# Optimization experiments

Measured on AMD Instinct MI355X. Metric: run time of the kernel, lower is better.

## Reference

```python
import jax, jax.numpy as jnp
import numpy as np

N = 50000      # nodes
E = 400000     # edges
F_NODE = 16    # node_features
F_EDGE = 8     # edge_features
H = 16         # hidden_dim
HID_MLP = 32   # edge-MLP hidden width (from MLP([edge_features, 32, ...]))
G = 64         # graphs in batch
T = 2          # num_targets
EPS = 1e-5


def setup_inputs() -> dict:
    key = jax.random.key(0)
    ks = jax.random.split(key, 16)
    def nrm(k, shape, s=0.05):
        return jax.random.normal(k, shape, jnp.float32) * s
    z = lambda *s: jnp.zeros(s, jnp.float32)
    o = lambda *s: jnp.ones(s, jnp.float32)
    inp = {}
    inp['x'] = jax.random.normal(ks[0], (N, F_NODE), jnp.float32)
    inp['edge_attr'] = jax.random.normal(ks[1], (E, F_EDGE), jnp.float32)
    # conv1 edge-MLP: Linear(F_EDGE,32) -> BN -> ReLU -> Linear(32, F_NODE*H)
    inp['e1_W1'] = nrm(ks[2], (F_EDGE, HID_MLP)); inp['e1_b1'] = z(HID_MLP)
    inp['e1_g'] = o(HID_MLP); inp['e1_be'] = z(HID_MLP)
    inp['e1_W2'] = nrm(ks[3], (HID_MLP, F_NODE * H)); inp['e1_b2'] = z(F_NODE * H)
    inp['c1_root'] = nrm(ks[4], (F_NODE, H)); inp['c1_bias'] = z(H)
    # conv2 edge-MLP: Linear(F_EDGE,32) -> BN -> ReLU -> Linear(32, H*H)
    inp['e2_W1'] = nrm(ks[5], (F_EDGE, HID_MLP)); inp['e2_b1'] = z(HID_MLP)
    inp['e2_g'] = o(HID_MLP); inp['e2_be'] = z(HID_MLP)
    inp['e2_W2'] = nrm(ks[6], (HID_MLP, H * H)); inp['e2_b2'] = z(H * H)
    inp['c2_root'] = nrm(ks[7], (H, H)); inp['c2_bias'] = z(H)
    # node batch norms
    inp['bn1_g'] = o(H); inp['bn1_b'] = z(H)
    inp['bn2_g'] = o(H); inp['bn2_b'] = z(H)
    # head MLP
    inp['fc1_W'] = nrm(ks[8], (H, H)); inp['fc1_b'] = z(H)
    inp['fc2_W'] = nrm(ks[9], (H, T)); inp['fc2_b'] = z(T)
    # int args
    inp['edge_index'] = jax.random.randint(ks[10], (2, E), 0, N, dtype=jnp.int32).astype(jnp.int64)
    inp['batch'] = jnp.sort(jax.random.randint(ks[11], (N,), 0, G, dtype=jnp.int32)).astype(jnp.int64)
    return inp


def _bn(h, g, b):
    # training-mode BatchNorm1d: batch stats, biased variance
    m = h.mean(0)
    v = jnp.mean((h - m) ** 2, axis=0)
    return g * (h - m) / jnp.sqrt(v + EPS) + b


def _edge_mlp(e, W1, b1, g, be, W2, b2):
    h = jax.nn.relu(_bn(e @ W1 + b1, g, be))
    return h @ W2 + b2


def _seg_mean(vals, idx, num):
    s = jax.ops.segment_sum(vals, idx, num_segments=num)
    c = jax.ops.segment_sum(jnp.ones((idx.shape[0],), vals.dtype), idx, num_segments=num)
    return s / jnp.maximum(c, 1.0)[:, None]


def _nnconv(x, src, dst, e, W1, b1, g, be, W2, b2, Wroot, bias, in_c, out_c):
    w = _edge_mlp(e, W1, b1, g, be, W2, b2).reshape(-1, in_c, out_c)  # [E, in, out]
    msg = jnp.einsum('ei,eio->eo', x[src], w)                        # gather + per-edge matmul
    agg = _seg_mean(msg, dst, x.shape[0])                            # scatter-mean into targets
    return agg + x @ Wroot + bias


def reference(x, edge_attr, e1_W1, e1_b1, e1_g, e1_be, e1_W2, e1_b2, c1_root, c1_bias,
              e2_W1, e2_b1, e2_g, e2_be, e2_W2, e2_b2, c2_root, c2_bias,
              bn1_g, bn1_b, bn2_g, bn2_b, fc1_W, fc1_b, fc2_W, fc2_b,
              edge_index, batch):
    src, dst = edge_index[0], edge_index[1]
    h = _nnconv(x, src, dst, edge_attr, e1_W1, e1_b1, e1_g, e1_be, e1_W2, e1_b2,
                c1_root, c1_bias, F_NODE, H)
    h = jax.nn.relu(_bn(h, bn1_g, bn1_b))
    h = _nnconv(h, src, dst, edge_attr, e2_W1, e2_b1, e2_g, e2_be, e2_W2, e2_b2,
                c2_root, c2_bias, H, H)
    h = jax.nn.relu(_bn(h, bn2_g, bn2_b))
    pooled = _seg_mean(h, batch, G)          # global_mean_pool -> [G, H]
    out = jax.nn.relu(pooled @ fc1_W + fc1_b) @ fc2_W + fc2_b
    return out
```

## Files before the change

### kernel.cpp

```cpp
#include <hip/hip_runtime.h>

#define N_NODES 50000
#define N_EDGES 400000
#define NG 64
#define NT 2
#define EPS 1e-5f
#define NB_N ((N_NODES + 255) / 256)
#define NB_E ((N_EDGES + 255) / 256)
#define NB_A ((N_NODES + 31) / 32)

constexpr int mom_i(int t) {
    int tt = t - 8; int i = 0;
    while (tt >= 8 - i) { tt -= 8 - i; ++i; }
    return i;
}
constexpr int mom_j(int t) {
    int tt = t - 8; int i = 0;
    while (tt >= 8 - i) { tt -= 8 - i; ++i; }
    return i + tt;
}

template<int IDX>
__device__ __forceinline__ float mom_term(const float* v) {
    if constexpr (IDX >= 44) return 0.f;
    else if constexpr (IDX < 8) return v[IDX];
    else return v[mom_i(IDX)] * v[mom_j(IDX)];
}

template<int BASE>
__device__ __forceinline__ void mom_add(const float* v, float* acc) {
    acc[0] += mom_term<BASE + 0>(v);
    acc[1] += mom_term<BASE + 1>(v);
    acc[2] += mom_term<BASE + 2>(v);
    acc[3] += mom_term<BASE + 3>(v);
    acc[4] += mom_term<BASE + 4>(v);
    acc[5] += mom_term<BASE + 5>(v);
    acc[6] += mom_term<BASE + 6>(v);
    acc[7] += mom_term<BASE + 7>(v);
}

template<int BASE>
__device__ __forceinline__ void mom_loop(
    const float* __restrict__ ea, const int* __restrict__ dst,
    int* __restrict__ deg, float* acc)
{
    const int stride = gridDim.x * 256;
    for (int e = blockIdx.x * 256 + threadIdx.x; e < N_EDGES; e += stride) {
        const float4 a4 = ((const float4*)ea)[e * 2];
        const float4 b4 = ((const float4*)ea)[e * 2 + 1];
        const float v[8] = {a4.x,a4.y,a4.z,a4.w, b4.x,b4.y,b4.z,b4.w};
        if constexpr (BASE == 0) atomicAdd(deg + dst[e], 1);
        mom_add<BASE>(v, acc);
    }
}

__global__ __launch_bounds__(256) void k_moments(
    const float* __restrict__ ea, const int* __restrict__ dst,
    float* __restrict__ mom, int* __restrict__ deg)
{
    const int c = blockIdx.y;
    float acc[8] = {0.f,0.f,0.f,0.f,0.f,0.f,0.f,0.f};
    switch (c) {
        case 0: mom_loop<0 >(ea, dst, deg, acc); break;
        case 1: mom_loop<8 >(ea, dst, deg, acc); break;
        case 2: mom_loop<16>(ea, dst, deg, acc); break;
        case 3: mom_loop<24>(ea, dst, deg, acc); break;
        case 4: mom_loop<32>(ea, dst, deg, acc); break;
        default: mom_loop<40>(ea, dst, deg, acc); break;
    }
    __shared__ float red[4][8];
    const int lane = threadIdx.x & 63, wv = threadIdx.x >> 6;
    #pragma unroll
    for (int u = 0; u < 8; ++u) {
        float s = acc[u];
        #pragma unroll
        for (int o = 32; o; o >>= 1) s += __shfl_down(s, o);
        if (lane == 0) red[wv][u] = s;
    }
    __syncthreads();
    if (threadIdx.x < 8) {
        const int idx = c * 8 + threadIdx.x;
        if (idx < 44) {
            const float s = red[0][threadIdx.x] + red[1][threadIdx.x]
                          + red[2][threadIdx.x] + red[3][threadIdx.x];
            atomicAdd(mom + idx, s);
        }
    }
}

__global__ __launch_bounds__(256) void k_scan1(
    const int* __restrict__ deg, int* __restrict__ loc, int* __restrict__ bsum,
    int* __restrict__ hist)
{
    __shared__ int s[256];
    __shared__ int shist[128];
    const int t = threadIdx.x;
    const int n = blockIdx.x * 256 + t;
    const int v = (n < N_NODES) ? deg[n] : 0;
    if (t < 128) shist[t] = 0;
    s[t] = v;
    __syncthreads();
    #pragma unroll
    for (int d = 1; d < 256; d <<= 1) {
        const int a = (t >= d) ? s[t - d] : 0;
        __syncthreads();
        s[t] += a;
        __syncthreads();
    }
    if (n < N_NODES) {
        loc[n] = s[t] - v;
        atomicAdd(&shist[min(v, 127)], 1);
    }
    if (t == 255) bsum[blockIdx.x] = s[t];
    __syncthreads();
    if (t < 128 && shist[t]) atomicAdd(hist + t, shist[t]);
}

__global__ __launch_bounds__(256) void k_singles(
    int* __restrict__ bsum, const float* __restrict__ mom,
    const float* __restrict__ W1a, const float* __restrict__ b1a,
    const float* __restrict__ ga,  const float* __restrict__ bea,
    const float* __restrict__ W1b, const float* __restrict__ b1b,
    const float* __restrict__ gb,  const float* __restrict__ beb,
    float* __restrict__ ss, const int* __restrict__ batch,
    int* __restrict__ start, const int* __restrict__ hist,
    int* __restrict__ cursor)
{
    __shared__ int s[256];
    const int t = threadIdx.x;
    const int v = (t < NB_N) ? bsum[t] : 0;
    s[t] = v;
    __syncthreads();
    #pragma unroll
    for (int d = 1; d < 256; d <<= 1) {
        const int a = (t >= d) ? s[t - d] : 0;
        __syncthreads();
        s[t] += a;
        __syncthreads();
    }
    if (t < NB_N) bsum[t] = s[t] - v;

    if (t < 64) {
        const int m = t >> 5, k = t & 31;
        const float* W1 = m ? W1b : W1a;
        const float b   = (m ? b1b : b1a)[k];
        const float g   = (m ? gb  : ga)[k];
        const float be  = (m ? beb : bea)[k];
        float w[8];
        #pragma unroll
        for (int j = 0; j < 8; ++j) w[j] = W1[j * 32 + k];
        float Sw = 0.f;
        #pragma unroll
        for (int j = 0; j < 8; ++j) Sw += mom[j] * w[j];
        float q = 0.f;
        int idx = 8;
        #pragma unroll
        for (int i = 0; i < 8; ++i)
            #pragma unroll
            for (int j = i; j < 8; ++j) {
                const float Mv = mom[idx++];
                q += Mv * w[i] * w[j] * (i == j ? 1.f : 2.f);
            }
        const float invE  = 1.0f / (float)N_EDGES;
        const float sump  = Sw + (float)N_EDGES * b;
        const float sumpp = q + 2.f * b * Sw + (float)N_EDGES * b * b;
        const float mean  = sump * invE;
        const float var   = fmaxf(sumpp * invE - mean * mean, 0.f);
        const float sc    = g * rsqrtf(var + EPS);
        ss[m * 64 + k]      = sc;
        ss[m * 64 + 32 + k] = be - mean * sc;
    }
    if (t <= NG) {
        int lo = 0, hi = N_NODES;
        while (lo < hi) {
            const int mid = (lo + hi) >> 1;
            if (batch[mid] < t) lo = mid + 1; else hi = mid;
        }
        start[t] = lo;
    }
    if (t == 0) {
        int acc = 0;
        for (int d = 127; d >= 0; --d) { cursor[d] = acc; acc += hist[d]; }
    }
}

__global__ __launch_bounds__(256) void k_scan3(
    const int* __restrict__ loc, const int* __restrict__ bsum,
    const int* __restrict__ deg, int* __restrict__ off, int* __restrict__ cur,
    int* __restrict__ cursor, int* __restrict__ perm)
{
    __shared__ int scnt[128];
    __shared__ int sbase[128];
    const int t = threadIdx.x;
    const int n = blockIdx.x * 256 + t;
    if (t < 128) scnt[t] = 0;
    __syncthreads();
    int b = 0, rk = 0;
    if (n < N_NODES) {
        const int o = loc[n] + bsum[n >> 8];
        off[n] = o; cur[n] = o;
        if (n == 0) off[N_NODES] = N_EDGES;
        b  = min(deg[n], 127);
        rk = atomicAdd(&scnt[b], 1);
    }
    __syncthreads();
    if (t < 128 && scnt[t]) sbase[t] = atomicAdd(cursor + t, scnt[t]);
    __syncthreads();
    if (n < N_NODES) perm[sbase[b] + rk] = n;
}

__global__ __launch_bounds__(256) void k_pos(
    const int* __restrict__ src, const int* __restrict__ dst,
    const float* __restrict__ ea, int* __restrict__ cur,
    int* __restrict__ src_s, float4* __restrict__ ea_s)
{
    const int e = blockIdx.x * 256 + threadIdx.x;
    if (e < N_EDGES) {
        const float4 a4 = ((const float4*)ea)[e * 2];
        const float4 b4 = ((const float4*)ea)[e * 2 + 1];
        const int p = atomicAdd(cur + dst[e], 1);
        src_s[p] = src[e];
        ea_s[p * 2]     = a4;
        ea_s[p * 2 + 1] = b4;
    }
}

__global__ __launch_bounds__(256) void k_agg(
    const float* __restrict__ x, const float4* __restrict__ ea_s,
    const int* __restrict__ src_s, const int* __restrict__ off,
    const int* __restrict__ perm,
    const float* __restrict__ W1, const float* __restrict__ W2,
    const float* __restrict__ ss,
    float* __restrict__ agg_out, float* __restrict__ xsum_out)
{
    __shared__ float4 sW2q[2048];
    const int tid = threadIdx.x;
    #pragma unroll
    for (int i = 0; i < 8; ++i) {
        const int f = tid + 256 * i;
        sW2q[f ^ ((f >> 8) & 7)] = ((const float4*)W2)[f];
    }
    __syncthreads();

    const int c  = tid & 7;
    const int g  = blockIdx.x * 32 + (tid >> 3);
    if (g >= N_NODES) return;
    const int n  = perm[g];

    float w1r[32];
    #pragma unroll
    for (int j = 0; j < 8; ++j)
        #pragma unroll
        for (int kk = 0; kk < 4; ++kk)
            w1r[j * 4 + kk] = W1[j * 32 + c * 4 + kk];
    float scr[4], shr[4];
    #pragma unroll
    for (int kk = 0; kk < 4; ++kk) {
        scr[kk] = ss[c * 4 + kk];
        shr[kk] = ss[32 + c * 4 + kk];
    }

    const int o0 = off[n], o1 = off[n + 1];
    float T[64];
    #pragma unroll
    for (int j = 0; j < 64; ++j) T[j] = 0.f;
    float xs0 = 0.f, xs1 = 0.f;

    float4 ca, cb, cx0, cx1, cx2, cx3;
    if (o0 < o1) {
        const int sn = src_s[o0];
        ca = ea_s[(size_t)o0 * 2];
        cb = ea_s[(size_t)o0 * 2 + 1];
        const float4* xp = (const float4*)(x + (size_t)sn * 16);
        cx0 = xp[0]; cx1 = xp[1]; cx2 = xp[2]; cx3 = xp[3];
    }
    for (int r = o0; r < o1; ++r) {
        float4 na = ca, nb = cb, nx0 = cx0, nx1 = cx1, nx2 = cx2, nx3 = cx3;
        if (r + 1 < o1) {
            const int sn = src_s[r + 1];
            na = ea_s[(size_t)(r + 1) * 2];
            nb = ea_s[(size_t)(r + 1) * 2 + 1];
            const float4* xp = (const float4*)(x + (size_t)sn * 16);
            nx0 = xp[0]; nx1 = xp[1]; nx2 = xp[2]; nx3 = xp[3];
        }
        const float ein[8] = {ca.x,ca.y,ca.z,ca.w, cb.x,cb.y,cb.z,cb.w};
        float h[4];
        #pragma unroll
        for (int kk = 0; kk < 4; ++kk) {
            float p = 0.f;
            #pragma unroll
            for (int j = 0; j < 8; ++j) p += ein[j] * w1r[j * 4 + kk];
            h[kk] = fmaxf(p * scr[kk] + shr[kk], 0.f);
        }
        const float xv[16] = {cx0.x,cx0.y,cx0.z,cx0.w, cx1.x,cx1.y,cx1.z,cx1.w,
                              cx2.x,cx2.y,cx2.z,cx2.w, cx3.x,cx3.y,cx3.z,cx3.w};
        #pragma unroll
        for (int kk = 0; kk < 4; ++kk) {
            const float hk = h[kk];
            #pragma unroll
            for (int i = 0; i < 16; ++i) T[kk * 16 + i] += hk * xv[i];
        }
        xs0 += xv[c * 2];
        xs1 += xv[c * 2 + 1];
        ca = na; cb = nb; cx0 = nx0; cx1 = nx1; cx2 = nx2; cx3 = nx3;
    }

    float agg[16];
    #pragma unroll
    for (int o = 0; o < 16; ++o) agg[o] = 0.f;
    #pragma unroll
    for (int kk = 0; kk < 4; ++kk) {
        const int fbase = (c * 4 + kk) * 64;
        #pragma unroll
        for (int i = 0; i < 16; ++i) {
            const float tv = T[kk * 16 + i];
            const int f0 = fbase + i * 4;
            const float4 w0 = sW2q[(f0 + 0) ^ c];
            const float4 w1 = sW2q[(f0 + 1) ^ c];
            const float4 w2 = sW2q[(f0 + 2) ^ c];
            const float4 w3 = sW2q[(f0 + 3) ^ c];
            agg[0]+=tv*w0.x; agg[1]+=tv*w0.y; agg[2]+=tv*w0.z; agg[3]+=tv*w0.w;
            agg[4]+=tv*w1.x; agg[5]+=tv*w1.y; agg[6]+=tv*w1.z; agg[7]+=tv*w1.w;
            agg[8]+=tv*w2.x; agg[9]+=tv*w2.y; agg[10]+=tv*w2.z; agg[11]+=tv*w2.w;
            agg[12]+=tv*w3.x; agg[13]+=tv*w3.y; agg[14]+=tv*w3.z; agg[15]+=tv*w3.w;
        }
    }
    #pragma unroll
    for (int m = 1; m < 8; m <<= 1) {
        #pragma unroll
        for (int o = 0; o < 16; ++o) agg[o] += __shfl_xor(agg[o], m);
    }
    ((float2*)(agg_out  + (size_t)n * 16))[c] = make_float2(agg[c * 2], agg[c * 2 + 1]);
    ((float2*)(xsum_out + (size_t)n * 16))[c] = make_float2(xs0, xs1);
}

__global__ __launch_bounds__(256) void k_node_pre(
    const float* __restrict__ agg, const float* __restrict__ xsum,
    const int* __restrict__ off, const float* __restrict__ xin,
    const float* __restrict__ root, const float* __restrict__ b2,
    const float* __restrict__ bias, float* __restrict__ bnstats,
    float* __restrict__ pre_out)
{
    __shared__ float sroot[256], sb2[256], sbias[16], lacc[32];
    const int tid = threadIdx.x;
    if (tid < 64) {
        ((float4*)sroot)[tid] = ((const float4*)root)[tid];
        ((float4*)sb2)[tid]   = ((const float4*)b2)[tid];
    }
    if (tid < 16) sbias[tid] = bias[tid];
    if (tid < 32) lacc[tid] = 0.f;
    __syncthreads();

    const int n = blockIdx.x * 256 + tid;
    const bool valid = (n < N_NODES);
    float pre[16];
    if (valid) {
        float acc[16];
        const float4* ap = (const float4*)(agg + (size_t)n * 16);
        const float4 a0 = ap[0], a1 = ap[1], a2 = ap[2], a3 = ap[3];
        acc[0]=a0.x; acc[1]=a0.y; acc[2]=a0.z; acc[3]=a0.w;
        acc[4]=a1.x; acc[5]=a1.y; acc[6]=a1.z; acc[7]=a1.w;
        acc[8]=a2.x; acc[9]=a2.y; acc[10]=a2.z; acc[11]=a2.w;
        acc[12]=a3.x; acc[13]=a3.y; acc[14]=a3.z; acc[15]=a3.w;
        const float4* sp = (const float4*)(xsum + (size_t)n * 16);
        const float4 s0 = sp[0], s1 = sp[1], s2 = sp[2], s3 = sp[3];
        const float sv[16] = {s0.x,s0.y,s0.z,s0.w, s1.x,s1.y,s1.z,s1.w,
                              s2.x,s2.y,s2.z,s2.w, s3.x,s3.y,s3.z,s3.w};
        #pragma unroll
        for (int i = 0; i < 16; ++i) {
            const float si = sv[i];
            #pragma unroll
            for (int o = 0; o < 16; ++o) acc[o] += si * sb2[i * 16 + o];
        }
        const float inv = 1.0f / (float)max(off[n + 1] - off[n], 1);
        const float4* xp = (const float4*)(xin + (size_t)n * 16);
        const float4 x0=xp[0],x1=xp[1],x2=xp[2],x3=xp[3];
        const float xn[16] = {x0.x,x0.y,x0.z,x0.w, x1.x,x1.y,x1.z,x1.w,
                              x2.x,x2.y,x2.z,x2.w, x3.x,x3.y,x3.z,x3.w};
        #pragma unroll
        for (int o = 0; o < 16; ++o) pre[o] = sbias[o] + acc[o] * inv;
        #pragma unroll
        for (int i = 0; i < 16; ++i) {
            const float xi = xn[i];
            #pragma unroll
            for (int o = 0; o < 16; ++o) pre[o] += xi * sroot[i * 16 + o];
        }
        float4* wp4 = (float4*)(pre_out + (size_t)n * 16);
        wp4[0] = make_float4(pre[0],pre[1],pre[2],pre[3]);
        wp4[1] = make_float4(pre[4],pre[5],pre[6],pre[7]);
        wp4[2] = make_float4(pre[8],pre[9],pre[10],pre[11]);
        wp4[3] = make_float4(pre[12],pre[13],pre[14],pre[15]);
    } else {
        #pragma unroll
        for (int o = 0; o < 16; ++o) pre[o] = 0.f;
    }
    const int lane = tid & 63;
    #pragma unroll
    for (int o = 0; o < 16; ++o) {
        float s = pre[o], q = s * s;
        #pragma unroll
        for (int w = 32; w; w >>= 1) {
            s += __shfl_down(s, w);
            q += __shfl_down(q, w);
        }
        if (lane == 0) { atomicAdd(&lacc[o], s); atomicAdd(&lacc[16 + o], q); }
    }
    __syncthreads();
    if (tid < 32) atomicAdd(bnstats + tid, lacc[tid]);
}

__global__ __launch_bounds__(256) void k_node_bn(
    const float* __restrict__ pre, const float* __restrict__ bnstats,
    const float* __restrict__ gam, const float* __restrict__ bet,
    float* __restrict__ hout)
{
    __shared__ float sscale[16], sshift[16];
    const int tid = threadIdx.x;
    if (tid < 16) {
        const float mean = bnstats[tid] * (1.0f / N_NODES);
        const float var  = fmaxf(bnstats[16 + tid] * (1.0f / N_NODES) - mean * mean, 0.f);
        const float rs   = rsqrtf(var + EPS);
        const float sc   = gam[tid] * rs;
        sscale[tid] = sc;
        sshift[tid] = bet[tid] - mean * sc;
    }
    __syncthreads();
    const int n = blockIdx.x * 256 + tid;
    if (n >= N_NODES) return;
    const float4* pp = (const float4*)(pre + (size_t)n * 16);
    const float4 p0=pp[0],p1=pp[1],p2=pp[2],p3=pp[3];
    const float pv[16] = {p0.x,p0.y,p0.z,p0.w, p1.x,p1.y,p1.z,p1.w,
                          p2.x,p2.y,p2.z,p2.w, p3.x,p3.y,p3.z,p3.w};
    float h[16];
    #pragma unroll
    for (int o = 0; o < 16; ++o) h[o] = fmaxf(pv[o] * sscale[o] + sshift[o], 0.f);
    float4* hp = (float4*)(hout + (size_t)n * 16);
    hp[0] = make_float4(h[0],h[1],h[2],h[3]);
    hp[1] = make_float4(h[4],h[5],h[6],h[7]);
    hp[2] = make_float4(h[8],h[9],h[10],h[11]);
    hp[3] = make_float4(h[12],h[13],h[14],h[15]);
}

__global__ __launch_bounds__(256) void k_pool_bn(
    const float* __restrict__ pre, const float* __restrict__ bnstats,
    const float* __restrict__ gam, const float* __restrict__ bet,
    const int* __restrict__ start, float* __restrict__ pool)
{
    __shared__ float lds[16][16];
    __shared__ float sscale[16], sshift[16];
    const int tid = threadIdx.x;
    if (tid < 16) {
        const float mean = bnstats[tid] * (1.0f / N_NODES);
        const float var  = fmaxf(bnstats[16 + tid] * (1.0f / N_NODES) - mean * mean, 0.f);
        const float rs   = rsqrtf(var + EPS);
        const float sc   = gam[tid] * rs;
        sscale[tid] = sc;
        sshift[tid] = bet[tid] - mean * sc;
    }
    __syncthreads();
    const int g = blockIdx.x;
    const int c = tid & 15, rg = tid >> 4;
    const int s = start[g], e = start[g + 1];
    const float sc = sscale[c], sh = sshift[c];
    float acc = 0.f;
    for (int r = s + rg; r < e; r += 16)
        acc += fmaxf(pre[(size_t)r * 16 + c] * sc + sh, 0.f);
    lds[rg][c] = acc;
    __syncthreads();
    if (tid < 16) {
        float sum = 0.f;
        #pragma unroll
        for (int i = 0; i < 16; ++i) sum += lds[i][tid];
        const float inv = 1.0f / (float)max(e - s, 1);
        pool[g * 16 + tid] = sum * inv;
    }
}

__global__ __launch_bounds__(64) void k_head(
    const float* __restrict__ pool,
    const float* __restrict__ fc1W, const float* __restrict__ fc1b,
    const float* __restrict__ fc2W, const float* __restrict__ fc2b,
    float* __restrict__ out)
{
    const int g = threadIdx.x;
    if (g >= NG) return;
    float p[16];
    #pragma unroll
    for (int o = 0; o < 16; ++o) p[o] = pool[g * 16 + o];
    float z[16];
    #pragma unroll
    for (int j = 0; j < 16; ++j) {
        float a = fc1b[j];
        #pragma unroll
        for (int o = 0; o < 16; ++o) a += p[o] * fc1W[o * 16 + j];
        z[j] = fmaxf(a, 0.f);
    }
    #pragma unroll
    for (int t = 0; t < NT; ++t) {
        float a = fc2b[t];
        #pragma unroll
        for (int j = 0; j < 16; ++j) a += z[j] * fc2W[j * 2 + t];
        out[g * 2 + t] = a;
    }
}

extern "C" void kernel_launch(void* const* d_in, const int* in_sizes, int n_in,
                              void* d_out, int out_size, void* d_ws, size_t ws_size,
                              hipStream_t stream)
{
    const float* x    = (const float*)d_in[0];
    const float* ea   = (const float*)d_in[1];
    const float* e1W1 = (const float*)d_in[2];  const float* e1b1 = (const float*)d_in[3];
    const float* e1g  = (const float*)d_in[4];  const float* e1be = (const float*)d_in[5];
    const float* e1W2 = (const float*)d_in[6];  const float* e1b2 = (const float*)d_in[7];
    const float* c1r  = (const float*)d_in[8];  const float* c1b  = (const float*)d_in[9];
    const float* e2W1 = (const float*)d_in[10]; const float* e2b1 = (const float*)d_in[11];
    const float* e2g  = (const float*)d_in[12]; const float* e2be = (const float*)d_in[13];
    const float* e2W2 = (const float*)d_in[14]; const float* e2b2 = (const float*)d_in[15];
    const float* c2r  = (const float*)d_in[16]; const float* c2b  = (const float*)d_in[17];
    const float* bn1g = (const float*)d_in[18]; const float* bn1b = (const float*)d_in[19];
    const float* bn2g = (const float*)d_in[20]; const float* bn2b = (const float*)d_in[21];
    const float* fc1W = (const float*)d_in[22]; const float* fc1b = (const float*)d_in[23];
    const float* fc2W = (const float*)d_in[24]; const float* fc2b = (const float*)d_in[25];
    const int* eidx   = (const int*)d_in[26];
    const int* batch  = (const int*)d_in[27];
    const int* src = eidx;
    const int* dst = eidx + N_EDGES;

    float* ws      = (float*)d_ws;
    float* mom     = ws;
    float* bnstats = ws + 64;
    float* ss      = ws + 128;
    int* hist_i    = (int*)(ws + 256);
    int* cursor_i  = (int*)(ws + 384);
    int* deg_i   = (int*)(ws + 512);
    int* loc_i   = deg_i + N_NODES;
    int* cur_i   = loc_i + N_NODES;
    int* bsum_i  = cur_i + N_NODES;
    int* start_i = bsum_i + 256;
    int* off_i   = start_i + 72;
    int* perm_i  = off_i + N_NODES + 8;
    int* src_s   = perm_i + N_NODES;
    const size_t fo = 512 + 256 + 72 + 8 + 5 * (size_t)N_NODES + (size_t)N_EDGES;
    float* ea_s  = ws + fo;
    float* aggb  = ea_s + (size_t)N_EDGES * 8;
    float* xsumb = aggb + (size_t)N_NODES * 16;
    float* pre1  = xsumb + (size_t)N_NODES * 16;
    float* h1n   = pre1 + (size_t)N_NODES * 16;
    float* pool  = h1n + (size_t)N_NODES * 16;

    hipMemsetAsync(d_ws, 0, (size_t)(512 + N_NODES) * sizeof(float), stream);

    k_moments<<<dim3(512, 6), 256, 0, stream>>>(ea, dst, mom, deg_i);
    k_scan1<<<NB_N, 256, 0, stream>>>(deg_i, loc_i, bsum_i, hist_i);
    k_singles<<<1, 256, 0, stream>>>(bsum_i, mom, e1W1, e1b1, e1g, e1be,
                                     e2W1, e2b1, e2g, e2be, ss, batch, start_i,
                                     hist_i, cursor_i);
    k_scan3<<<NB_N, 256, 0, stream>>>(loc_i, bsum_i, deg_i, off_i, cur_i,
                                      cursor_i, perm_i);
    k_pos<<<NB_E, 256, 0, stream>>>(src, dst, ea, cur_i, src_s, (float4*)ea_s);

    k_agg<<<NB_A, 256, 0, stream>>>(x, (const float4*)ea_s, src_s, off_i, perm_i,
                                    e1W1, e1W2, ss, aggb, xsumb);
    k_node_pre<<<NB_N, 256, 0, stream>>>(aggb, xsumb, off_i, x, c1r, e1b2,
                                         c1b, bnstats, pre1);
    k_node_bn<<<NB_N, 256, 0, stream>>>(pre1, bnstats, bn1g, bn1b, h1n);

    k_agg<<<NB_A, 256, 0, stream>>>(h1n, (const float4*)ea_s, src_s, off_i, perm_i,
                                    e2W1, e2W2, ss + 64, aggb, xsumb);
    k_node_pre<<<NB_N, 256, 0, stream>>>(aggb, xsumb, off_i, h1n, c2r, e2b2,
                                         c2b, bnstats + 32, pre1);

    k_pool_bn<<<NG, 256, 0, stream>>>(pre1, bnstats + 32, bn2g, bn2b, start_i, pool);
    k_head<<<1, 64, 0, stream>>>(pool, fc1W, fc1b, fc2W, fc2b, (float*)d_out);
}
```

Before: 252.5 us.

## Process two nodes per thread group in k_agg and halve moment-kernel grid

k_agg now has each 8-lane group handle two consecutive (degree-sorted) nodes, running two edge loops and sharing each shared-memory W2 read across both nodes' contractions. This halves the block count and amortizes the W2 staging and LDS reads. The cost is doubled accumulator registers (two 64-float T arrays), with launch_bounds(256,1) allowing heavy register use at the risk of lower occupancy and less latency hiding for the gathers. The moments kernel also accumulates 16 moment terms per thread instead of 8, so it launches 3 grid rows instead of 6 and reads edge_attr fewer times.

```diff
diff --git a/kernel.cpp b/kernel.cpp
--- a/kernel.cpp
+++ b/kernel.cpp
@@ -7,7 +7,7 @@
 #define EPS 1e-5f
 #define NB_N ((N_NODES + 255) / 256)
 #define NB_E ((N_EDGES + 255) / 256)
-#define NB_A ((N_NODES + 31) / 32)
+#define NB_A2 ((N_NODES + 63) / 64)
 
 constexpr int mom_i(int t) {
     int tt = t - 8; int i = 0;
@@ -28,15 +28,23 @@
 }
 
 template<int BASE>
-__device__ __forceinline__ void mom_add(const float* v, float* acc) {
-    acc[0] += mom_term<BASE + 0>(v);
-    acc[1] += mom_term<BASE + 1>(v);
-    acc[2] += mom_term<BASE + 2>(v);
-    acc[3] += mom_term<BASE + 3>(v);
-    acc[4] += mom_term<BASE + 4>(v);
-    acc[5] += mom_term<BASE + 5>(v);
-    acc[6] += mom_term<BASE + 6>(v);
-    acc[7] += mom_term<BASE + 7>(v);
+__device__ __forceinline__ void mom_add16(const float* v, float* acc) {
+    acc[0]  += mom_term<BASE + 0>(v);
+    acc[1]  += mom_term<BASE + 1>(v);
+    acc[2]  += mom_term<BASE + 2>(v);
+    acc[3]  += mom_term<BASE + 3>(v);
+    acc[4]  += mom_term<BASE + 4>(v);
+    acc[5]  += mom_term<BASE + 5>(v);
+    acc[6]  += mom_term<BASE + 6>(v);
+    acc[7]  += mom_term<BASE + 7>(v);
+    acc[8]  += mom_term<BASE + 8>(v);
+    acc[9]  += mom_term<BASE + 9>(v);
+    acc[10] += mom_term<BASE + 10>(v);
+    acc[11] += mom_term<BASE + 11>(v);
+    acc[12] += mom_term<BASE + 12>(v);
+    acc[13] += mom_term<BASE + 13>(v);
+    acc[14] += mom_term<BASE + 14>(v);
+    acc[15] += mom_term<BASE + 15>(v);
 }
 
 template<int BASE>
@@ -50,7 +58,7 @@
         const float4 b4 = ((const float4*)ea)[e * 2 + 1];
         const float v[8] = {a4.x,a4.y,a4.z,a4.w, b4.x,b4.y,b4.z,b4.w};
         if constexpr (BASE == 0) atomicAdd(deg + dst[e], 1);
-        mom_add<BASE>(v, acc);
+        mom_add16<BASE>(v, acc);
     }
 }
 
@@ -59,27 +67,26 @@
     float* __restrict__ mom, int* __restrict__ deg)
 {
     const int c = blockIdx.y;
-    float acc[8] = {0.f,0.f,0.f,0.f,0.f,0.f,0.f,0.f};
+    float acc[16];
+    #pragma unroll
+    for (int u = 0; u < 16; ++u) acc[u] = 0.f;
     switch (c) {
         case 0: mom_loop<0 >(ea, dst, deg, acc); break;
-        case 1: mom_loop<8 >(ea, dst, deg, acc); break;
-        case 2: mom_loop<16>(ea, dst, deg, acc); break;
-        case 3: mom_loop<24>(ea, dst, deg, acc); break;
-        case 4: mom_loop<32>(ea, dst, deg, acc); break;
-        default: mom_loop<40>(ea, dst, deg, acc); break;
-    }
-    __shared__ float red[4][8];
+        case 1: mom_loop<16>(ea, dst, deg, acc); break;
+        default: mom_loop<32>(ea, dst, deg, acc); break;
+    }
+    __shared__ float red[4][16];
     const int lane = threadIdx.x & 63, wv = threadIdx.x >> 6;
     #pragma unroll
-    for (int u = 0; u < 8; ++u) {
+    for (int u = 0; u < 16; ++u) {
         float s = acc[u];
         #pragma unroll
         for (int o = 32; o; o >>= 1) s += __shfl_down(s, o);
         if (lane == 0) red[wv][u] = s;
     }
     __syncthreads();
-    if (threadIdx.x < 8) {
-        const int idx = c * 8 + threadIdx.x;
+    if (threadIdx.x < 16) {
+        const int idx = c * 16 + threadIdx.x;
         if (idx < 44) {
             const float s = red[0][threadIdx.x] + red[1][threadIdx.x]
                           + red[2][threadIdx.x] + red[3][threadIdx.x];
@@ -225,7 +232,49 @@
     }
 }
 
-__global__ __launch_bounds__(256) void k_agg(
+#define EDGE_LOOP(Tarr, XS0, XS1, O0, O1)                                      \
+    {                                                                          \
+        float4 ca, cb, cx0, cx1, cx2, cx3;                                     \
+        if ((O0) < (O1)) {                                                     \
+            const int sn = src_s[(O0)];                                        \
+            ca = ea_s[(size_t)(O0) * 2];                                       \
+            cb = ea_s[(size_t)(O0) * 2 + 1];                                   \
+            const float4* xp = (const float4*)(x + (size_t)sn * 16);           \
+            cx0 = xp[0]; cx1 = xp[1]; cx2 = xp[2]; cx3 = xp[3];                \
+        }                                                                      \
+        for (int r = (O0); r < (O1); ++r) {                                    \
+            float4 na = ca, nb = cb, nx0 = cx0, nx1 = cx1, nx2 = cx2, nx3 = cx3;\
+            if (r + 1 < (O1)) {                                                \
+                const int sn = src_s[r + 1];                                   \
+                na = ea_s[(size_t)(r + 1) * 2];                                \
+                nb = ea_s[(size_t)(r + 1) * 2 + 1];                            \
+                const float4* xp = (const float4*)(x + (size_t)sn * 16);       \
+                nx0 = xp[0]; nx1 = xp[1]; nx2 = xp[2]; nx3 = xp[3];            \
+            }                                                                  \
+            const float ein[8] = {ca.x,ca.y,ca.z,ca.w, cb.x,cb.y,cb.z,cb.w};   \
+            float h[4];                                                        \
+            _Pragma("unroll")                                                  \
+            for (int kk = 0; kk < 4; ++kk) {                                   \
+                float p = 0.f;                                                 \
+                _Pragma("unroll")                                              \
+                for (int j = 0; j < 8; ++j) p += ein[j] * w1r[j * 4 + kk];     \
+                h[kk] = fmaxf(p * scr[kk] + shr[kk], 0.f);                     \
+            }                                                                  \
+            const float xv[16] = {cx0.x,cx0.y,cx0.z,cx0.w, cx1.x,cx1.y,cx1.z,cx1.w,\
+                                  cx2.x,cx2.y,cx2.z,cx2.w, cx3.x,cx3.y,cx3.z,cx3.w};\
+            _Pragma("unroll")                                                  \
+            for (int kk = 0; kk < 4; ++kk) {                                   \
+                const float hk = h[kk];                                        \
+                _Pragma("unroll")                                              \
+                for (int i = 0; i < 16; ++i) Tarr[kk * 16 + i] += hk * xv[i];  \
+            }                                                                  \
+            XS0 += xv[c * 2];                                                  \
+            XS1 += xv[c * 2 + 1];                                              \
+            ca = na; cb = nb; cx0 = nx0; cx1 = nx1; cx2 = nx2; cx3 = nx3;      \
+        }                                                                      \
+    }
+
+__global__ __launch_bounds__(256, 1) void k_agg(
     const float* __restrict__ x, const float4* __restrict__ ea_s,
     const int* __restrict__ src_s, const int* __restrict__ off,
     const int* __restrict__ perm,
@@ -243,9 +292,11 @@
     __syncthreads();
 
     const int c  = tid & 7;
-    const int g  = blockIdx.x * 32 + (tid >> 3);
+    const int g  = blockIdx.x * 64 + (tid >> 3) * 2;
     if (g >= N_NODES) return;
-    const int n  = perm[g];
+    const int nA = perm[g];
+    const bool hasB = (g + 1 < N_NODES);
+    const int nB = hasB ? perm[g + 1] : nA;
 
     float w1r[32];
     #pragma unroll
@@ -260,78 +311,56 @@
         shr[kk] = ss[32 + c * 4 + kk];
     }
 
-    const int o0 = off[n], o1 = off[n + 1];
-    float T[64];
-    #pragma unroll
-    for (int j = 0; j < 64; ++j) T[j] = 0.f;
-    float xs0 = 0.f, xs1 = 0.f;
-
-    float4 ca, cb, cx0, cx1, cx2, cx3;
-    if (o0 < o1) {
-        const int sn = src_s[o0];
-        ca = ea_s[(size_t)o0 * 2];
-        cb = ea_s[(size_t)o0 * 2 + 1];
-        const float4* xp = (const float4*)(x + (size_t)sn * 16);
-        cx0 = xp[0]; cx1 = xp[1]; cx2 = xp[2]; cx3 = xp[3];
-    }
-    for (int r = o0; r < o1; ++r) {
-        float4 na = ca, nb = cb, nx0 = cx0, nx1 = cx1, nx2 = cx2, nx3 = cx3;
-        if (r + 1 < o1) {
-            const int sn = src_s[r + 1];
-            na = ea_s[(size_t)(r + 1) * 2];
-            nb = ea_s[(size_t)(r + 1) * 2 + 1];
-            const float4* xp = (const float4*)(x + (size_t)sn * 16);
-            nx0 = xp[0]; nx1 = xp[1]; nx2 = xp[2]; nx3 = xp[3];
-        }
-        const float ein[8] = {ca.x,ca.y,ca.z,ca.w, cb.x,cb.y,cb.z,cb.w};
-        float h[4];
-        #pragma unroll
-        for (int kk = 0; kk < 4; ++kk) {
-            float p = 0.f;
-            #pragma unroll
-            for (int j = 0; j < 8; ++j) p += ein[j] * w1r[j * 4 + kk];
-            h[kk] = fmaxf(p * scr[kk] + shr[kk], 0.f);
-        }
-        const float xv[16] = {cx0.x,cx0.y,cx0.z,cx0.w, cx1.x,cx1.y,cx1.z,cx1.w,
-                              cx2.x,cx2.y,cx2.z,cx2.w, cx3.x,cx3.y,cx3.z,cx3.w};
-        #pragma unroll
-        for (int kk = 0; kk < 4; ++kk) {
-            const float hk = h[kk];
-            #pragma unroll
-            for (int i = 0; i < 16; ++i) T[kk * 16 + i] += hk * xv[i];
-        }
-        xs0 += xv[c * 2];
-        xs1 += xv[c * 2 + 1];
-        ca = na; cb = nb; cx0 = nx0; cx1 = nx1; cx2 = nx2; cx3 = nx3;
-    }
-
-    float agg[16];
-    #pragma unroll
-    for (int o = 0; o < 16; ++o) agg[o] = 0.f;
+    const int a0 = off[nA], a1 = off[nA + 1];
+    const int b0 = hasB ? off[nB] : 0, b1 = hasB ? off[nB + 1] : 0;
+
+    float TA[64], TB[64];
+    #pragma unroll
+    for (int j = 0; j < 64; ++j) { TA[j] = 0.f; TB[j] = 0.f; }
+    float xsA0 = 0.f, xsA1 = 0.f, xsB0 = 0.f, xsB1 = 0.f;
+
+    EDGE_LOOP(TA, xsA0, xsA1, a0, a1)
+    EDGE_LOOP(TB, xsB0, xsB1, b0, b1)
+
+    float aggA[16], aggB[16];
+    #pragma unroll
+    for (int o = 0; o < 16; ++o) { aggA[o] = 0.f; aggB[o] = 0.f; }
     #pragma unroll
     for (int kk = 0; kk < 4; ++kk) {
         const int fbase = (c * 4 + kk) * 64;
         #pragma unroll
         for (int i = 0; i < 16; ++i) {
-            const float tv = T[kk * 16 + i];
+            const float ta = TA[kk * 16 + i];
+            const float tb = TB[kk * 16 + i];
             const int f0 = fbase + i * 4;
             const float4 w0 = sW2q[(f0 + 0) ^ c];
             const float4 w1 = sW2q[(f0 + 1) ^ c];
             const float4 w2 = sW2q[(f0 + 2) ^ c];
             const float4 w3 = sW2q[(f0 + 3) ^ c];
-            agg[0]+=tv*w0.x; agg[1]+=tv*w0.y; agg[2]+=tv*w0.z; agg[3]+=tv*w0.w;
-            agg[4]+=tv*w1.x; agg[5]+=tv*w1.y; agg[6]+=tv*w1.z; agg[7]+=tv*w1.w;
-            agg[8]+=tv*w2.x; agg[9]+=tv*w2.y; agg[10]+=tv*w2.z; agg[11]+=tv*w2.w;
-            agg[12]+=tv*w3.x; agg[13]+=tv*w3.y; agg[14]+=tv*w3.z; agg[15]+=tv*w3.w;
+            aggA[0]+=ta*w0.x; aggA[1]+=ta*w0.y; aggA[2]+=ta*w0.z; aggA[3]+=ta*w0.w;
+            aggA[4]+=ta*w1.x; aggA[5]+=ta*w1.y; aggA[6]+=ta*w1.z; aggA[7]+=ta*w1.w;
+            aggA[8]+=ta*w2.x; aggA[9]+=ta*w2.y; aggA[10]+=ta*w2.z; aggA[11]+=ta*w2.w;
+            aggA[12]+=ta*w3.x; aggA[13]+=ta*w3.y; aggA[14]+=ta*w3.z; aggA[15]+=ta*w3.w;
+            aggB[0]+=tb*w0.x; aggB[1]+=tb*w0.y; aggB[2]+=tb*w0.z; aggB[3]+=tb*w0.w;
+            aggB[4]+=tb*w1.x; aggB[5]+=tb*w1.y; aggB[6]+=tb*w1.z; aggB[7]+=tb*w1.w;
+            aggB[8]+=tb*w2.x; aggB[9]+=tb*w2.y; aggB[10]+=tb*w2.z; aggB[11]+=tb*w2.w;
+            aggB[12]+=tb*w3.x; aggB[13]+=tb*w3.y; aggB[14]+=tb*w3.z; aggB[15]+=tb*w3.w;
         }
     }
     #pragma unroll
     for (int m = 1; m < 8; m <<= 1) {
         #pragma unroll
-        for (int o = 0; o < 16; ++o) agg[o] += __shfl_xor(agg[o], m);
-    }
-    ((float2*)(agg_out  + (size_t)n * 16))[c] = make_float2(agg[c * 2], agg[c * 2 + 1]);
-    ((float2*)(xsum_out + (size_t)n * 16))[c] = make_float2(xs0, xs1);
+        for (int o = 0; o < 16; ++o) {
+            aggA[o] += __shfl_xor(aggA[o], m);
+            aggB[o] += __shfl_xor(aggB[o], m);
+        }
+    }
+    ((float2*)(agg_out  + (size_t)nA * 16))[c] = make_float2(aggA[c*2], aggA[c*2+1]);
+    ((float2*)(xsum_out + (size_t)nA * 16))[c] = make_float2(xsA0, xsA1);
+    if (hasB) {
+        ((float2*)(agg_out  + (size_t)nB * 16))[c] = make_float2(aggB[c*2], aggB[c*2+1]);
+        ((float2*)(xsum_out + (size_t)nB * 16))[c] = make_float2(xsB0, xsB1);
+    }
 }
 
 __global__ __launch_bounds__(256) void k_node_pre(
@@ -551,7 +580,7 @@
 
     hipMemsetAsync(d_ws, 0, (size_t)(512 + N_NODES) * sizeof(float), stream);
 
-    k_moments<<<dim3(512, 6), 256, 0, stream>>>(ea, dst, mom, deg_i);
+    k_moments<<<dim3(512, 3), 256, 0, stream>>>(ea, dst, mom, deg_i);
     k_scan1<<<NB_N, 256, 0, stream>>>(deg_i, loc_i, bsum_i, hist_i);
     k_singles<<<1, 256, 0, stream>>>(bsum_i, mom, e1W1, e1b1, e1g, e1be,
                                      e2W1, e2b1, e2g, e2be, ss, batch, start_i,
@@ -560,14 +589,14 @@
                                       cursor_i, perm_i);
     k_pos<<<NB_E, 256, 0, stream>>>(src, dst, ea, cur_i, src_s, (float4*)ea_s);
 
-    k_agg<<<NB_A, 256, 0, stream>>>(x, (const float4*)ea_s, src_s, off_i, perm_i,
-                                    e1W1, e1W2, ss, aggb, xsumb);
+    k_agg<<<NB_A2, 256, 0, stream>>>(x, (const float4*)ea_s, src_s, off_i, perm_i,
+                                     e1W1, e1W2, ss, aggb, xsumb);
     k_node_pre<<<NB_N, 256, 0, stream>>>(aggb, xsumb, off_i, x, c1r, e1b2,
                                          c1b, bnstats, pre1);
     k_node_bn<<<NB_N, 256, 0, stream>>>(pre1, bnstats, bn1g, bn1b, h1n);
 
-    k_agg<<<NB_A, 256, 0, stream>>>(h1n, (const float4*)ea_s, src_s, off_i, perm_i,
-                                    e2W1, e2W2, ss + 64, aggb, xsumb);
+    k_agg<<<NB_A2, 256, 0, stream>>>(h1n, (const float4*)ea_s, src_s, off_i, perm_i,
+                                     e2W1, e2W2, ss + 64, aggb, xsumb);
     k_node_pre<<<NB_N, 256, 0, stream>>>(aggb, xsumb, off_i, h1n, c2r, e2b2,
                                          c2b, bnstats + 32, pre1);
 
```

Result: slower. 289.4 us (+14.6%).
